# Performance work log

Hardware: AMD Instinct MI355X
Metric: run time of the kernel (lower is better)

## Reference

```python
import jax, jax.numpy as jnp
import numpy as np

N_INST = 64  # number of distinct instance colors generated (color = 4*label, label 0 = background)
LAMBDA_SEP = 300.0


def setup_inputs() -> dict:
    key = jax.random.key(0)
    k1, k2 = jax.random.split(key)
    B, H, W = 4, 768, 768
    labels = jax.random.randint(k1, (B, H, W), 0, N_INST)
    labels = labels.at[:, :8, :8].set(0)  # guarantee background pixels exist (torch code assumes bg_pred is set)
    # target colors: (4*l, 4*l, 4*l) in [0, 252]; background label 0 -> (0,0,0)
    target = jnp.broadcast_to((labels * 4).astype(jnp.float32)[:, None, :, :], (B, 3, H, W))
    prediction = jax.random.uniform(k2, (B, 3, H, W), dtype=jnp.float32) * 255.0
    no_bg = jnp.zeros((B,), dtype=bool)
    return {"prediction": prediction, "target": target, "no_bg": no_bg}


def _huber(x, c):
    # elementwise huber, delta=1.0 (torch default)
    d = jnp.abs(x - c)
    return jnp.where(d < 1.0, 0.5 * d * d, d - 0.5)


def _per_image(P, L, nobg):
    # P: [N,3] predicted colors, L: [N] int instance labels (0 = background)
    N = P.shape[0]
    counts = jax.ops.segment_sum(jnp.ones((N,), P.dtype), L, num_segments=N_INST)  # [K]
    safe = jnp.maximum(counts, 1.0)
    means = jax.ops.segment_sum(P, L, num_segments=N_INST) / safe[:, None]  # [K,3]
    # intra-instance huber toward constant target (255 for instances, 0 for background), mean over 3*count elems
    h255 = _huber(P, 255.0).sum(-1)  # [N]
    h0 = _huber(P, 0.0).sum(-1)
    var = jax.ops.segment_sum(h255, L, num_segments=N_INST) / (3.0 * safe)
    var0 = jax.ops.segment_sum(h0, L, num_segments=N_INST) / (3.0 * safe)
    var = var.at[0].set(var0[0])
    # pixel -> instance-mean squared distances [N,K] (separation term)
    D = jnp.sum((P[:, None, :] - means[None, :, :]) ** 2, axis=-1)
    inv = LAMBDA_SEP / (1.0 + D)  # [N,K]
    bg_mask = (L == 0).astype(P.dtype)  # [N]
    bg_cnt = bg_mask.sum()
    nbg_cnt = jnp.asarray(N, P.dtype) - bg_cnt
    # non-bg instance k: mean over background pixels of 300/(1+||p - mean_k||^2)
    sep = (bg_mask @ inv) / jnp.maximum(bg_cnt, 1.0)  # [K]
    # background instance: mean over non-background pixels vs bg mean
    sep0 = ((1.0 - bg_mask) @ inv[:, 0]) / jnp.maximum(nbg_cnt, 1.0)
    sep = sep.at[0].set(sep0)
    w = 10.0 / jnp.sqrt(safe)
    present = counts > 0
    included = present.at[0].set(jnp.logical_and(present[0], jnp.logical_not(nobg)))
    incl = included.astype(P.dtype)
    ct = jnp.maximum(incl.sum(), 1.0)
    return jnp.sum(incl * (var + w * sep)) / ct


def reference(prediction, target, no_bg):
    B = prediction.shape[0]
    # recover integer instance labels from color map (generation: color = 4*label on all 3 channels)
    labels = jnp.round(target[:, 0] / 4.0).astype(jnp.int32).reshape(B, -1)  # [B,N]
    P = jnp.transpose(prediction, (0, 2, 3, 1)).reshape(B, -1, 3)  # [B,N,3]
    losses = jax.vmap(_per_image)(P, labels, no_bg)
    return jnp.mean(losses)
```

## Files before the change

### kernel.cpp

```cpp
#include <hip/hip_runtime.h>

#define NINST 64
#define ACC_STRIDE 512
#define OFF_CNT  0
#define OFF_SUM  64
#define OFF_H255 256
#define OFF_H0   320
#define LAMBDA_SEP 300.0f

#define P1_GX 128
#define P1_THREADS 512
#define P1_WAVES (P1_THREADS / 64)
#define P2_GX 128
#define P3_GX 32
#define P3_TILE 256
#define CNT_STRIDE 64
#define BGBUF 512

__device__ __forceinline__ float huber1(float x, float c) {
    float d = fabsf(x - c);
    return d < 1.0f ? 0.5f * d * d : d - 0.5f;
}

__global__ __launch_bounds__(P1_THREADS, 4)
void k_pass1(const float* __restrict__ pred, const float* __restrict__ targ,
             float* __restrict__ acc, unsigned* __restrict__ bgcnt,
             float* __restrict__ bglist, int maxbg, int N) {
    __shared__ float4 s_stage[P1_WAVES][256];
    __shared__ float4 s_red[P1_WAVES][NINST];
    __shared__ float s_corr255[NINST];
    __shared__ float s_corr0;
    __shared__ float s_bgbuf[BGBUF * 3];
    __shared__ unsigned s_bgn;
    __shared__ unsigned s_base;
    int tid = threadIdx.x;
    int lane = tid & 63;
    int wv = tid >> 6;
    int grp = lane >> 3;
    int s8 = (lane & 7) << 3;
    if (tid < NINST) s_corr255[tid] = 0.0f;
    if (tid == 0) { s_corr0 = 0.0f; s_bgn = 0u; }
    __syncthreads();

    int b = blockIdx.y;
    const float* bp = pred + (size_t)b * 3 * N;
    const float* bt = targ + (size_t)b * 3 * N;
    const float4* t0 = (const float4*)bt;
    const float4* p0 = (const float4*)bp;
    const float4* p1 = (const float4*)(bp + N);
    const float4* p2 = (const float4*)(bp + 2 * N);
    unsigned* bgc = &bgcnt[(size_t)b * CNT_STRIDE];
    float* bgl = bglist + (size_t)b * maxbg * 3;
    float* g = acc + (size_t)b * ACC_STRIDE;

    float cnt[8], sx[8], sy[8], sz[8];
#pragma unroll
    for (int t = 0; t < 8; t++) { cnt[t] = 0.0f; sx[t] = 0.0f; sy[t] = 0.0f; sz[t] = 0.0f; }

    int M = N >> 2;
    int stride = gridDim.x * blockDim.x;
    for (int base = blockIdx.x * blockDim.x + wv * 64; base < M; base += stride) {
        int i = base + lane;
        float xx[4], yy[4], zz[4];
        int labs[4];
        if (i < M) {
            float4 t = t0[i], a = p0[i], c = p1[i], d = p2[i];
            float tt[4] = {t.x, t.y, t.z, t.w};
            xx[0] = a.x; xx[1] = a.y; xx[2] = a.z; xx[3] = a.w;
            yy[0] = c.x; yy[1] = c.y; yy[2] = c.z; yy[3] = c.w;
            zz[0] = d.x; zz[1] = d.y; zz[2] = d.z; zz[3] = d.w;
#pragma unroll
            for (int j = 0; j < 4; j++) {
                int lab = (int)(tt[j] * 0.25f + 0.5f);
                labs[j] = lab;
                float dx = 255.0f - xx[j], dy = 255.0f - yy[j], dz = 255.0f - zz[j];
                float corr = 0.0f;
                if (dx < 1.0f) { float e = 1.0f - dx; corr += 0.5f * e * e; }
                if (dy < 1.0f) { float e = 1.0f - dy; corr += 0.5f * e * e; }
                if (dz < 1.0f) { float e = 1.0f - dz; corr += 0.5f * e * e; }
                if (corr != 0.0f) atomicAdd(&s_corr255[lab], corr);
                if (lab == 0) {
                    float c0 = 0.0f;
                    if (xx[j] < 1.0f) { float e = 1.0f - xx[j]; c0 += 0.5f * e * e; }
                    if (yy[j] < 1.0f) { float e = 1.0f - yy[j]; c0 += 0.5f * e * e; }
                    if (zz[j] < 1.0f) { float e = 1.0f - zz[j]; c0 += 0.5f * e * e; }
                    if (c0 != 0.0f) atomicAdd(&s_corr0, c0);
                    unsigned idx = atomicAdd(&s_bgn, 1u);
                    if (idx < BGBUF) {
                        s_bgbuf[idx * 3 + 0] = xx[j];
                        s_bgbuf[idx * 3 + 1] = yy[j];
                        s_bgbuf[idx * 3 + 2] = zz[j];
                    } else {
                        unsigned gi = atomicAdd(bgc, 1u);
                        if ((int)gi < maxbg) {
                            bgl[(size_t)gi * 3 + 0] = xx[j];
                            bgl[(size_t)gi * 3 + 1] = yy[j];
                            bgl[(size_t)gi * 3 + 2] = zz[j];
                        }
                    }
                }
            }
        } else {
#pragma unroll
            for (int j = 0; j < 4; j++) { xx[j] = yy[j] = zz[j] = 0.0f; labs[j] = -1; }
        }
#pragma unroll
        for (int j = 0; j < 4; j++)
            s_stage[wv][j * 64 + lane] =
                make_float4(xx[j], yy[j], zz[j], __int_as_float(labs[j]));
#pragma unroll 4
        for (int j = 0; j < 32; j++) {
            float4 v = s_stage[wv][(j << 3) + grp];
            int rel = __float_as_int(v.w) - s8;
#pragma unroll
            for (int t = 0; t < 8; t++) {
                float m = (rel == t) ? 1.0f : 0.0f;
                cnt[t] += m;
                sx[t] = fmaf(m, v.x, sx[t]);
                sy[t] = fmaf(m, v.y, sy[t]);
                sz[t] = fmaf(m, v.z, sz[t]);
            }
        }
    }

#pragma unroll
    for (int q = 0; q < 4; q++)
        s_stage[wv][(lane << 2) + q] = make_float4(cnt[q], sx[q], sy[q], sz[q]);
    __syncthreads();
    {
        int l = lane & 31;
        float4 ra = make_float4(0.0f, 0.0f, 0.0f, 0.0f);
#pragma unroll
        for (int gg = 0; gg < 8; gg++) {
            float4 p = s_stage[wv][gg * 32 + l];
            ra.x += p.x; ra.y += p.y; ra.z += p.z; ra.w += p.w;
        }
        if (lane < 32) s_red[wv][((l >> 2) << 3) + (l & 3)] = ra;
    }
    __syncthreads();
#pragma unroll
    for (int q = 0; q < 4; q++)
        s_stage[wv][(lane << 2) + q] = make_float4(cnt[q + 4], sx[q + 4], sy[q + 4], sz[q + 4]);
    __syncthreads();
    {
        int l = lane & 31;
        float4 rb = make_float4(0.0f, 0.0f, 0.0f, 0.0f);
#pragma unroll
        for (int gg = 0; gg < 8; gg++) {
            float4 p = s_stage[wv][gg * 32 + l];
            rb.x += p.x; rb.y += p.y; rb.z += p.z; rb.w += p.w;
        }
        if (lane >= 32) s_red[wv][((l >> 2) << 3) + 4 + (l & 3)] = rb;
    }
    __syncthreads();

    unsigned nloc = s_bgn < (unsigned)BGBUF ? s_bgn : (unsigned)BGBUF;
    if (tid == 0) s_base = atomicAdd(bgc, nloc);
    __syncthreads();
    {
        unsigned base3 = s_base * 3u;
        unsigned lim3 = (unsigned)maxbg * 3u;
        for (unsigned i = tid; i < nloc * 3u; i += blockDim.x) {
            if (base3 + i < lim3) bgl[base3 + i] = s_bgbuf[i];
        }
    }

    if (tid < NINST) {
        float c = 0.0f, x = 0.0f, y = 0.0f, z = 0.0f;
#pragma unroll
        for (int w = 0; w < P1_WAVES; w++) {
            float4 r = s_red[w][tid];
            c += r.x; x += r.y; y += r.z; z += r.w;
        }
        float s3 = x + y + z;
        atomicAdd(&g[OFF_CNT + tid], c);
        atomicAdd(&g[OFF_SUM + tid * 3 + 0], x);
        atomicAdd(&g[OFF_SUM + tid * 3 + 1], y);
        atomicAdd(&g[OFF_SUM + tid * 3 + 2], z);
        atomicAdd(&g[OFF_H255 + tid], 763.5f * c - s3 + s_corr255[tid]);
        if (tid == 0) atomicAdd(&g[OFF_H0], s3 - 1.5f * c + s_corr0);
    }

    if (blockIdx.x == 0 && tid < (N & 3)) {
        int i = (M << 2) + tid;
        float t = bt[i], x = bp[i], y = bp[N + i], z = bp[2 * N + i];
        int lab = (int)(t * 0.25f + 0.5f);
        atomicAdd(&g[OFF_CNT + lab], 1.0f);
        atomicAdd(&g[OFF_SUM + lab * 3 + 0], x);
        atomicAdd(&g[OFF_SUM + lab * 3 + 1], y);
        atomicAdd(&g[OFF_SUM + lab * 3 + 2], z);
        atomicAdd(&g[OFF_H255 + lab], huber1(x, 255.f) + huber1(y, 255.f) + huber1(z, 255.f));
        if (lab == 0) {
            atomicAdd(&g[OFF_H0], huber1(x, 0.f) + huber1(y, 0.f) + huber1(z, 0.f));
            unsigned gi = atomicAdd(bgc, 1u);
            if ((int)gi < maxbg) {
                bgl[(size_t)gi * 3 + 0] = x;
                bgl[(size_t)gi * 3 + 1] = y;
                bgl[(size_t)gi * 3 + 2] = z;
            }
        }
    }
}

__global__ void k_pass2(const float* __restrict__ pred, const float* __restrict__ targ,
                        const float* __restrict__ acc, float* __restrict__ p2part, int N) {
    __shared__ float s_w[16];
    int tid = threadIdx.x;
    int b = blockIdx.y;
    const float* g = acc + (size_t)b * ACC_STRIDE;
    float safe0 = fmaxf(g[OFF_CNT + 0], 1.0f);
    float m0x = g[OFF_SUM + 0] / safe0;
    float m0y = g[OFF_SUM + 1] / safe0;
    float m0z = g[OFF_SUM + 2] / safe0;

    const float* base_p = pred + (size_t)b * 3 * N;
    const float* base_t = targ + (size_t)b * 3 * N;
    const float4* p0 = (const float4*)(base_p);
    const float4* p1 = (const float4*)(base_p + N);
    const float4* p2 = (const float4*)(base_p + 2 * N);
    const float4* t0 = (const float4*)(base_t);

    float local = 0.0f;
    int M = N >> 2;
    for (int i = blockIdx.x * blockDim.x + tid; i < M; i += gridDim.x * blockDim.x) {
        float4 t = t0[i], a = p0[i], c = p1[i], d = p2[i];
        float ts[4] = {t.x, t.y, t.z, t.w};
        float xs[4] = {a.x, a.y, a.z, a.w};
        float ys[4] = {c.x, c.y, c.z, c.w};
        float zs[4] = {d.x, d.y, d.z, d.w};
#pragma unroll
        for (int j = 0; j < 4; j++) {
            float dx = xs[j] - m0x, dy = ys[j] - m0y, dz = zs[j] - m0z;
            float D = dx * dx + dy * dy + dz * dz;
            float m = (ts[j] > 2.0f) ? LAMBDA_SEP : 0.0f;
            local = fmaf(m, __builtin_amdgcn_rcpf(1.0f + D), local);
        }
    }
    if (blockIdx.x == 0) {
        for (int i = (M << 2) + tid; i < N; i += blockDim.x) {
            float dx = base_p[i] - m0x, dy = base_p[N + i] - m0y, dz = base_p[2 * N + i] - m0z;
            float D = dx * dx + dy * dy + dz * dz;
            float m = (base_t[i] > 2.0f) ? LAMBDA_SEP : 0.0f;
            local = fmaf(m, __builtin_amdgcn_rcpf(1.0f + D), local);
        }
    }
#pragma unroll
    for (int o = 32; o > 0; o >>= 1) local += __shfl_down(local, o, 64);
    int wv = tid >> 6;
    if ((tid & 63) == 0) s_w[wv] = local;
    __syncthreads();
    if (tid == 0) {
        float s = 0.0f;
        int nw = blockDim.x >> 6;
        for (int i = 0; i < nw; i++) s += s_w[i];
        p2part[(size_t)b * P2_GX + blockIdx.x] = s;
    }
}

__global__ void k_pass3(const float* __restrict__ bglist, const unsigned* __restrict__ bgcnt,
                        const float* __restrict__ acc, float* __restrict__ p3part, int maxbg) {
    __shared__ float s_px[P3_TILE * 3];
    __shared__ float s_part[4][NINST];
    int tid = threadIdx.x;
    int lane = tid & 63;
    int wv = tid >> 6;
    int b = blockIdx.y;
    const float* g = acc + (size_t)b * ACC_STRIDE;
    float safe = fmaxf(g[OFF_CNT + lane], 1.0f);
    float mx = g[OFF_SUM + lane * 3 + 0] / safe;
    float my = g[OFF_SUM + lane * 3 + 1] / safe;
    float mz = g[OFF_SUM + lane * 3 + 2] / safe;

    int nb = min((int)bgcnt[(size_t)b * CNT_STRIDE], maxbg);
    const float* bgl = bglist + (size_t)b * maxbg * 3;

    float lacc = 0.0f;
    int ntiles = (nb + P3_TILE - 1) / P3_TILE;
    for (int tile = blockIdx.x; tile < ntiles; tile += gridDim.x) {
        int base = tile * P3_TILE;
        int cnt = min(P3_TILE, nb - base);
        __syncthreads();
        for (int i = tid; i < cnt * 3; i += blockDim.x) s_px[i] = bgl[(size_t)base * 3 + i];
        __syncthreads();
        int lim = cnt - wv * 64;
        lim = lim < 0 ? 0 : (lim > 64 ? 64 : lim);
        const float* px = &s_px[wv * 64 * 3];
        for (int j = 0; j < lim; j++) {
            float x = px[j * 3 + 0];
            float y = px[j * 3 + 1];
            float z = px[j * 3 + 2];
            float dx = x - mx, dy = y - my, dz = z - mz;
            float D = dx * dx + dy * dy + dz * dz;
            lacc += LAMBDA_SEP * __builtin_amdgcn_rcpf(1.0f + D);
        }
    }
    s_part[wv][lane] = lacc;
    __syncthreads();
    if (tid < NINST) {
        p3part[((size_t)b * P3_GX + blockIdx.x) * NINST + tid] =
            s_part[0][tid] + s_part[1][tid] + s_part[2][tid] + s_part[3][tid];
    }
}

__global__ void k_final(const float* __restrict__ acc, const float* __restrict__ p2part,
                        const float* __restrict__ p3part, const unsigned char* __restrict__ nobg,
                        float* __restrict__ out, int N, int B) {
    int tid = threadIdx.x;
    float total = 0.0f;
    for (int b = 0; b < B; b++) {
        const float* g = acc + (size_t)b * ACC_STRIDE;
        float c = g[OFF_CNT + tid];
        float c0 = g[OFF_CNT + 0];
        bool incl = (c > 0.0f);
        if (tid == 0 && nobg[b] != 0) incl = false;
        float safe = fmaxf(c, 1.0f);
        float var = (tid == 0 ? g[OFF_H0] : g[OFF_H255 + tid]) / (3.0f * safe);
        float sepnum;
        if (tid == 0) {
            float s = 0.0f;
            for (int i = 0; i < P2_GX; i++) s += p2part[(size_t)b * P2_GX + i];
            sepnum = s;
        } else {
            float s = 0.0f;
#pragma unroll
            for (int j = 0; j < P3_GX; j++) s += p3part[((size_t)b * P3_GX + j) * NINST + tid];
            sepnum = s;
        }
        float denom = (tid == 0) ? fmaxf((float)N - c0, 1.0f) : fmaxf(c0, 1.0f);
        float sep = sepnum / denom;
        float w = 10.0f / sqrtf(safe);
        float term = incl ? (var + w * sep) : 0.0f;
        float cnt = incl ? 1.0f : 0.0f;
#pragma unroll
        for (int o = 32; o > 0; o >>= 1) {
            term += __shfl_down(term, o, 64);
            cnt += __shfl_down(cnt, o, 64);
        }
        if (tid == 0) total += term / fmaxf(cnt, 1.0f);
    }
    if (tid == 0) out[0] = total / (float)B;
}

extern "C" void kernel_launch(void* const* d_in, const int* in_sizes, int n_in,
                              void* d_out, int out_size, void* d_ws, size_t ws_size,
                              hipStream_t stream) {
    const float* pred = (const float*)d_in[0];
    const float* targ = (const float*)d_in[1];
    const unsigned char* nobg = (const unsigned char*)d_in[2];
    float* out = (float*)d_out;

    int B = in_sizes[2];
    int N = in_sizes[0] / (3 * B);

    float* acc = (float*)d_ws;
    size_t acc_bytes = (size_t)B * ACC_STRIDE * sizeof(float);
    unsigned* bgcnt = (unsigned*)((char*)d_ws + acc_bytes);
    size_t head = acc_bytes + 4096;
    float* p2part = (float*)((char*)d_ws + head);
    size_t p2_bytes = (size_t)B * P2_GX * sizeof(float);
    float* p3part = p2part + (size_t)B * P2_GX;
    size_t p3_bytes = (size_t)B * P3_GX * NINST * sizeof(float);
    size_t list_off = head + p2_bytes + p3_bytes;
    list_off = (list_off + 255) & ~(size_t)255;
    float* bglist = (float*)((char*)d_ws + list_off);

    int maxbg = 0;
    if (ws_size > list_off) {
        size_t cap = (ws_size - list_off) / ((size_t)B * 3 * sizeof(float));
        maxbg = (int)(cap < (size_t)131072 ? cap : (size_t)131072);
    }

    hipMemsetAsync(d_ws, 0, head, stream);

    dim3 g1(P1_GX, B);
    k_pass1<<<g1, dim3(P1_THREADS), 0, stream>>>(pred, targ, acc, bgcnt, bglist, maxbg, N);
    dim3 g2(P2_GX, B);
    k_pass2<<<g2, dim3(1024), 0, stream>>>(pred, targ, acc, p2part, N);
    dim3 g3(P3_GX, B);
    k_pass3<<<g3, dim3(256), 0, stream>>>(bglist, bgcnt, acc, p3part, maxbg);
    k_final<<<dim3(1), dim3(64), 0, stream>>>(acc, p2part, p3part, nobg, out, N, B);
}
```

Baseline: 78.55 us.

## Fuse pass2 and pass3 into one launch and prefetch loads in pass1

Pass 2 (background-mean separation over all pixels) and pass 3 (instance separation over background pixels) become a single kernel whose grid is split by block index, so one launch and its gap disappear. Pass 3 now uses 8 blocks of 1024 threads with larger tiles instead of 32 blocks of 256. Pass 1 gets a register double-buffer that loads the next iteration's float4s before computing the current one, runs more blocks, and reindexes its shared-memory reduction. The final kernel reduces the 128 pass-2 partials with a wave shuffle instead of a serial loop. Fewer pass-3 blocks may leave that work less parallel, and the prefetch adds register pressure.

```diff
diff --git a/kernel.cpp b/kernel.cpp
--- a/kernel.cpp
+++ b/kernel.cpp
@@ -8,12 +8,13 @@
 #define OFF_H0   320
 #define LAMBDA_SEP 300.0f
 
-#define P1_GX 128
+#define P1_GX 192
 #define P1_THREADS 512
 #define P1_WAVES (P1_THREADS / 64)
 #define P2_GX 128
-#define P3_GX 32
-#define P3_TILE 256
+#define P23_THREADS 1024
+#define P3B 8
+#define P3_TILE 1024
 #define CNT_STRIDE 64
 #define BGBUF 512
 
@@ -59,16 +60,31 @@
 
     int M = N >> 2;
     int stride = gridDim.x * blockDim.x;
-    for (int base = blockIdx.x * blockDim.x + wv * 64; base < M; base += stride) {
+    int base = blockIdx.x * blockDim.x + wv * 64;
+
+    float4 ct = make_float4(0, 0, 0, 0), ca = ct, cc = ct, cd = ct;
+    if (base < M) {
         int i = base + lane;
+        if (i < M) { ct = t0[i]; ca = p0[i]; cc = p1[i]; cd = p2[i]; }
+    }
+
+    for (; base < M;) {
+        int i = base + lane;
+        bool valid = i < M;
+        int nbase = base + stride;
+        float4 nt = make_float4(0, 0, 0, 0), na = nt, nc = nt, nd = nt;
+        if (nbase < M) {
+            int ni = nbase + lane;
+            if (ni < M) { nt = t0[ni]; na = p0[ni]; nc = p1[ni]; nd = p2[ni]; }
+        }
+
         float xx[4], yy[4], zz[4];
         int labs[4];
-        if (i < M) {
-            float4 t = t0[i], a = p0[i], c = p1[i], d = p2[i];
-            float tt[4] = {t.x, t.y, t.z, t.w};
-            xx[0] = a.x; xx[1] = a.y; xx[2] = a.z; xx[3] = a.w;
-            yy[0] = c.x; yy[1] = c.y; yy[2] = c.z; yy[3] = c.w;
-            zz[0] = d.x; zz[1] = d.y; zz[2] = d.z; zz[3] = d.w;
+        if (valid) {
+            float tt[4] = {ct.x, ct.y, ct.z, ct.w};
+            xx[0] = ca.x; xx[1] = ca.y; xx[2] = ca.z; xx[3] = ca.w;
+            yy[0] = cc.x; yy[1] = cc.y; yy[2] = cc.z; yy[3] = cc.w;
+            zz[0] = cd.x; zz[1] = cd.y; zz[2] = cd.z; zz[3] = cd.w;
 #pragma unroll
             for (int j = 0; j < 4; j++) {
                 int lab = (int)(tt[j] * 0.25f + 0.5f);
@@ -121,36 +137,37 @@
                 sz[t] = fmaf(m, v.z, sz[t]);
             }
         }
+        base = nbase; ct = nt; ca = na; cc = nc; cd = nd;
     }
 
 #pragma unroll
     for (int q = 0; q < 4; q++)
-        s_stage[wv][(lane << 2) + q] = make_float4(cnt[q], sx[q], sy[q], sz[q]);
-    __syncthreads();
-    {
-        int l = lane & 31;
+        s_stage[wv][q * 64 + lane] = make_float4(cnt[q], sx[q], sy[q], sz[q]);
+    __syncthreads();
+    if (lane < 32) {
+        int s = lane & 7, q = lane >> 3;
         float4 ra = make_float4(0.0f, 0.0f, 0.0f, 0.0f);
 #pragma unroll
         for (int gg = 0; gg < 8; gg++) {
-            float4 p = s_stage[wv][gg * 32 + l];
+            float4 p = s_stage[wv][q * 64 + (gg << 3) + s];
             ra.x += p.x; ra.y += p.y; ra.z += p.z; ra.w += p.w;
         }
-        if (lane < 32) s_red[wv][((l >> 2) << 3) + (l & 3)] = ra;
+        s_red[wv][(s << 3) + q] = ra;
     }
     __syncthreads();
 #pragma unroll
     for (int q = 0; q < 4; q++)
-        s_stage[wv][(lane << 2) + q] = make_float4(cnt[q + 4], sx[q + 4], sy[q + 4], sz[q + 4]);
-    __syncthreads();
-    {
-        int l = lane & 31;
+        s_stage[wv][q * 64 + lane] = make_float4(cnt[q + 4], sx[q + 4], sy[q + 4], sz[q + 4]);
+    __syncthreads();
+    if (lane < 32) {
+        int s = lane & 7, q = lane >> 3;
         float4 rb = make_float4(0.0f, 0.0f, 0.0f, 0.0f);
 #pragma unroll
         for (int gg = 0; gg < 8; gg++) {
-            float4 p = s_stage[wv][gg * 32 + l];
+            float4 p = s_stage[wv][q * 64 + (gg << 3) + s];
             rb.x += p.x; rb.y += p.y; rb.z += p.z; rb.w += p.w;
         }
-        if (lane >= 32) s_red[wv][((l >> 2) << 3) + 4 + (l & 3)] = rb;
+        s_red[wv][(s << 3) + q + 4] = rb;
     }
     __syncthreads();
 
@@ -202,103 +219,104 @@
     }
 }
 
-__global__ void k_pass2(const float* __restrict__ pred, const float* __restrict__ targ,
-                        const float* __restrict__ acc, float* __restrict__ p2part, int N) {
+__global__ void k_pass23(const float* __restrict__ pred, const float* __restrict__ targ,
+                         const float* __restrict__ acc, const float* __restrict__ bglist,
+                         const unsigned* __restrict__ bgcnt, float* __restrict__ p2part,
+                         float* __restrict__ p3part, int maxbg, int N) {
     __shared__ float s_w[16];
+    __shared__ float s_px[P3_TILE * 3];
+    __shared__ float s_part[16][NINST];
     int tid = threadIdx.x;
     int b = blockIdx.y;
     const float* g = acc + (size_t)b * ACC_STRIDE;
-    float safe0 = fmaxf(g[OFF_CNT + 0], 1.0f);
-    float m0x = g[OFF_SUM + 0] / safe0;
-    float m0y = g[OFF_SUM + 1] / safe0;
-    float m0z = g[OFF_SUM + 2] / safe0;
-
-    const float* base_p = pred + (size_t)b * 3 * N;
-    const float* base_t = targ + (size_t)b * 3 * N;
-    const float4* p0 = (const float4*)(base_p);
-    const float4* p1 = (const float4*)(base_p + N);
-    const float4* p2 = (const float4*)(base_p + 2 * N);
-    const float4* t0 = (const float4*)(base_t);
-
-    float local = 0.0f;
-    int M = N >> 2;
-    for (int i = blockIdx.x * blockDim.x + tid; i < M; i += gridDim.x * blockDim.x) {
-        float4 t = t0[i], a = p0[i], c = p1[i], d = p2[i];
-        float ts[4] = {t.x, t.y, t.z, t.w};
-        float xs[4] = {a.x, a.y, a.z, a.w};
-        float ys[4] = {c.x, c.y, c.z, c.w};
-        float zs[4] = {d.x, d.y, d.z, d.w};
-#pragma unroll
-        for (int j = 0; j < 4; j++) {
-            float dx = xs[j] - m0x, dy = ys[j] - m0y, dz = zs[j] - m0z;
-            float D = dx * dx + dy * dy + dz * dz;
-            float m = (ts[j] > 2.0f) ? LAMBDA_SEP : 0.0f;
-            local = fmaf(m, __builtin_amdgcn_rcpf(1.0f + D), local);
-        }
-    }
-    if (blockIdx.x == 0) {
-        for (int i = (M << 2) + tid; i < N; i += blockDim.x) {
-            float dx = base_p[i] - m0x, dy = base_p[N + i] - m0y, dz = base_p[2 * N + i] - m0z;
-            float D = dx * dx + dy * dy + dz * dz;
-            float m = (base_t[i] > 2.0f) ? LAMBDA_SEP : 0.0f;
-            local = fmaf(m, __builtin_amdgcn_rcpf(1.0f + D), local);
-        }
-    }
-#pragma unroll
-    for (int o = 32; o > 0; o >>= 1) local += __shfl_down(local, o, 64);
-    int wv = tid >> 6;
-    if ((tid & 63) == 0) s_w[wv] = local;
-    __syncthreads();
-    if (tid == 0) {
-        float s = 0.0f;
-        int nw = blockDim.x >> 6;
-        for (int i = 0; i < nw; i++) s += s_w[i];
-        p2part[(size_t)b * P2_GX + blockIdx.x] = s;
-    }
-}
-
-__global__ void k_pass3(const float* __restrict__ bglist, const unsigned* __restrict__ bgcnt,
-                        const float* __restrict__ acc, float* __restrict__ p3part, int maxbg) {
-    __shared__ float s_px[P3_TILE * 3];
-    __shared__ float s_part[4][NINST];
-    int tid = threadIdx.x;
-    int lane = tid & 63;
-    int wv = tid >> 6;
-    int b = blockIdx.y;
-    const float* g = acc + (size_t)b * ACC_STRIDE;
-    float safe = fmaxf(g[OFF_CNT + lane], 1.0f);
-    float mx = g[OFF_SUM + lane * 3 + 0] / safe;
-    float my = g[OFF_SUM + lane * 3 + 1] / safe;
-    float mz = g[OFF_SUM + lane * 3 + 2] / safe;
-
-    int nb = min((int)bgcnt[(size_t)b * CNT_STRIDE], maxbg);
-    const float* bgl = bglist + (size_t)b * maxbg * 3;
-
-    float lacc = 0.0f;
-    int ntiles = (nb + P3_TILE - 1) / P3_TILE;
-    for (int tile = blockIdx.x; tile < ntiles; tile += gridDim.x) {
-        int base = tile * P3_TILE;
-        int cnt = min(P3_TILE, nb - base);
+
+    if (blockIdx.x < P2_GX) {
+        float safe0 = fmaxf(g[OFF_CNT + 0], 1.0f);
+        float m0x = g[OFF_SUM + 0] / safe0;
+        float m0y = g[OFF_SUM + 1] / safe0;
+        float m0z = g[OFF_SUM + 2] / safe0;
+
+        const float* base_p = pred + (size_t)b * 3 * N;
+        const float* base_t = targ + (size_t)b * 3 * N;
+        const float4* p0 = (const float4*)(base_p);
+        const float4* p1 = (const float4*)(base_p + N);
+        const float4* p2 = (const float4*)(base_p + 2 * N);
+        const float4* t0 = (const float4*)(base_t);
+
+        float local = 0.0f;
+        int M = N >> 2;
+        for (int i = blockIdx.x * blockDim.x + tid; i < M; i += P2_GX * blockDim.x) {
+            float4 t = t0[i], a = p0[i], c = p1[i], d = p2[i];
+            float ts[4] = {t.x, t.y, t.z, t.w};
+            float xs[4] = {a.x, a.y, a.z, a.w};
+            float ys[4] = {c.x, c.y, c.z, c.w};
+            float zs[4] = {d.x, d.y, d.z, d.w};
+#pragma unroll
+            for (int j = 0; j < 4; j++) {
+                float dx = xs[j] - m0x, dy = ys[j] - m0y, dz = zs[j] - m0z;
+                float D = dx * dx + dy * dy + dz * dz;
+                float m = (ts[j] > 2.0f) ? LAMBDA_SEP : 0.0f;
+                local = fmaf(m, __builtin_amdgcn_rcpf(1.0f + D), local);
+            }
+        }
+        if (blockIdx.x == 0) {
+            for (int i = (M << 2) + tid; i < N; i += blockDim.x) {
+                float dx = base_p[i] - m0x, dy = base_p[N + i] - m0y, dz = base_p[2 * N + i] - m0z;
+                float D = dx * dx + dy * dy + dz * dz;
+                float m = (base_t[i] > 2.0f) ? LAMBDA_SEP : 0.0f;
+                local = fmaf(m, __builtin_amdgcn_rcpf(1.0f + D), local);
+            }
+        }
+#pragma unroll
+        for (int o = 32; o > 0; o >>= 1) local += __shfl_down(local, o, 64);
+        int wv = tid >> 6;
+        if ((tid & 63) == 0) s_w[wv] = local;
         __syncthreads();
-        for (int i = tid; i < cnt * 3; i += blockDim.x) s_px[i] = bgl[(size_t)base * 3 + i];
+        if (tid == 0) {
+            float s = 0.0f;
+            for (int i = 0; i < (P23_THREADS >> 6); i++) s += s_w[i];
+            p2part[(size_t)b * P2_GX + blockIdx.x] = s;
+        }
+    } else {
+        int bx = blockIdx.x - P2_GX;
+        int lane = tid & 63;
+        int wv = tid >> 6;
+        float safe = fmaxf(g[OFF_CNT + lane], 1.0f);
+        float mx = g[OFF_SUM + lane * 3 + 0] / safe;
+        float my = g[OFF_SUM + lane * 3 + 1] / safe;
+        float mz = g[OFF_SUM + lane * 3 + 2] / safe;
+
+        int nb = min((int)bgcnt[(size_t)b * CNT_STRIDE], maxbg);
+        const float* bgl = bglist + (size_t)b * maxbg * 3;
+
+        float lacc = 0.0f;
+        int ntiles = (nb + P3_TILE - 1) / P3_TILE;
+        for (int tile = bx; tile < ntiles; tile += P3B) {
+            int base = tile * P3_TILE;
+            int cnt = min(P3_TILE, nb - base);
+            __syncthreads();
+            for (int i = tid; i < cnt * 3; i += blockDim.x) s_px[i] = bgl[(size_t)base * 3 + i];
+            __syncthreads();
+            int lim = cnt - wv * 64;
+            lim = lim < 0 ? 0 : (lim > 64 ? 64 : lim);
+            const float* px = &s_px[wv * 64 * 3];
+            for (int j = 0; j < lim; j++) {
+                float x = px[j * 3 + 0];
+                float y = px[j * 3 + 1];
+                float z = px[j * 3 + 2];
+                float dx = x - mx, dy = y - my, dz = z - mz;
+                float D = dx * dx + dy * dy + dz * dz;
+                lacc += LAMBDA_SEP * __builtin_amdgcn_rcpf(1.0f + D);
+            }
+        }
+        s_part[wv][lane] = lacc;
         __syncthreads();
-        int lim = cnt - wv * 64;
-        lim = lim < 0 ? 0 : (lim > 64 ? 64 : lim);
-        const float* px = &s_px[wv * 64 * 3];
-        for (int j = 0; j < lim; j++) {
-            float x = px[j * 3 + 0];
-            float y = px[j * 3 + 1];
-            float z = px[j * 3 + 2];
-            float dx = x - mx, dy = y - my, dz = z - mz;
-            float D = dx * dx + dy * dy + dz * dz;
-            lacc += LAMBDA_SEP * __builtin_amdgcn_rcpf(1.0f + D);
-        }
-    }
-    s_part[wv][lane] = lacc;
-    __syncthreads();
-    if (tid < NINST) {
-        p3part[((size_t)b * P3_GX + blockIdx.x) * NINST + tid] =
-            s_part[0][tid] + s_part[1][tid] + s_part[2][tid] + s_part[3][tid];
+        if (tid < NINST) {
+            float s = 0.0f;
+#pragma unroll
+            for (int w = 0; w < 16; w++) s += s_part[w][tid];
+            p3part[((size_t)b * P3B + bx) * NINST + tid] = s;
+        }
     }
 }
 
@@ -315,15 +333,16 @@
         if (tid == 0 && nobg[b] != 0) incl = false;
         float safe = fmaxf(c, 1.0f);
         float var = (tid == 0 ? g[OFF_H0] : g[OFF_H255 + tid]) / (3.0f * safe);
+        float s2 = p2part[(size_t)b * P2_GX + tid] + p2part[(size_t)b * P2_GX + NINST + tid];
+#pragma unroll
+        for (int o = 32; o > 0; o >>= 1) s2 += __shfl_down(s2, o, 64);
         float sepnum;
         if (tid == 0) {
-            float s = 0.0f;
-            for (int i = 0; i < P2_GX; i++) s += p2part[(size_t)b * P2_GX + i];
-            sepnum = s;
+            sepnum = s2;
         } else {
             float s = 0.0f;
 #pragma unroll
-            for (int j = 0; j < P3_GX; j++) s += p3part[((size_t)b * P3_GX + j) * NINST + tid];
+            for (int j = 0; j < P3B; j++) s += p3part[((size_t)b * P3B + j) * NINST + tid];
             sepnum = s;
         }
         float denom = (tid == 0) ? fmaxf((float)N - c0, 1.0f) : fmaxf(c0, 1.0f);
@@ -359,7 +378,7 @@
     float* p2part = (float*)((char*)d_ws + head);
     size_t p2_bytes = (size_t)B * P2_GX * sizeof(float);
     float* p3part = p2part + (size_t)B * P2_GX;
-    size_t p3_bytes = (size_t)B * P3_GX * NINST * sizeof(float);
+    size_t p3_bytes = (size_t)B * P3B * NINST * sizeof(float);
     size_t list_off = head + p2_bytes + p3_bytes;
     list_off = (list_off + 255) & ~(size_t)255;
     float* bglist = (float*)((char*)d_ws + list_off);
@@ -374,9 +393,8 @@
 
     dim3 g1(P1_GX, B);
     k_pass1<<<g1, dim3(P1_THREADS), 0, stream>>>(pred, targ, acc, bgcnt, bglist, maxbg, N);
-    dim3 g2(P2_GX, B);
-    k_pass2<<<g2, dim3(1024), 0, stream>>>(pred, targ, acc, p2part, N);
-    dim3 g3(P3_GX, B);
-    k_pass3<<<g3, dim3(256), 0, stream>>>(bglist, bgcnt, acc, p3part, maxbg);
+    dim3 g23(P2_GX + P3B, B);
+    k_pass23<<<g23, dim3(P23_THREADS), 0, stream>>>(pred, targ, acc, bglist, bgcnt,
+                                                    p2part, p3part, maxbg, N);
     k_final<<<dim3(1), dim3(64), 0, stream>>>(acc, p2part, p3part, nobg, out, N, B);
 }
```

After: 79.11 us. No clear change (+0.7%).
